# Optimization experiments

Measured on AMD Instinct MI355X. Metric: run time of the kernel, lower is better.

## Reference

```python
import jax, jax.numpy as jnp
import numpy as np

B, N, T, E = 8, 10000, 12, 160000
C_IN, C_SP, C_OUT, K = 32, 64, 64, 3
EPS = 1e-5

def _conv1xk(x, w, b, pad):
    # x: (B, Cin, N, T), w: (Cout, Cin, 1, k) -- conv only along time axis
    y = jax.lax.conv_general_dilated(x, w, (1, 1), [(0, 0), (pad, pad)],
                                     dimension_numbers=('NCHW', 'OIHW', 'NCHW'))
    return y + b[None, :, None, None]

def _temporal_block(x, w, b, gamma, beta, mean, var):
    out = _conv1xk(x, w, b, pad=1)
    p, q = jnp.split(out, 2, axis=1)
    out = p * jax.nn.sigmoid(q)  # GLU gate
    scale = gamma * jax.lax.rsqrt(var + EPS)  # eval-mode BatchNorm2d
    return (out - mean[None, :, None, None]) * scale[None, :, None, None] + beta[None, :, None, None]

def _cheb_conv(x, edge_index, edge_weight, W, b):
    # x: (BT, N, C). PyG ChebConv, sym normalization, lambda_max=2 =>
    # Lhat = -D^{-1/2} A D^{-1/2} (zero diagonal). Recursion T0=x, T1=Lhat x,
    # Tk = 2 Lhat T_{k-1} - T_{k-2}; out = sum_k Tk @ W_k + b.
    row, col = edge_index[0], edge_index[1]
    n = x.shape[1]
    deg = jnp.zeros((n,), x.dtype).at[row].add(edge_weight)
    deg_safe = jnp.where(deg > 0, deg, 1.0)
    dinv = jnp.where(deg > 0, jax.lax.rsqrt(deg_safe), 0.0)
    norm = -edge_weight * dinv[row] * dinv[col]  # (E,)

    def lhat(z):
        msg = z[:, row, :] * norm[None, :, None]          # gather + scale
        return jnp.zeros_like(z).at[:, col, :].add(msg)   # scatter-add

    Tx0 = x
    out = jnp.einsum('bnc,cd->bnd', Tx0, W[0])
    Tx1 = lhat(x)
    out = out + jnp.einsum('bnc,cd->bnd', Tx1, W[1])
    for k in range(2, W.shape[0]):
        Tx2 = 2.0 * lhat(Tx1) - Tx0
        out = out + jnp.einsum('bnc,cd->bnd', Tx2, W[k])
        Tx0, Tx1 = Tx1, Tx2
    return out + b

def setup_inputs():
    key = jax.random.key(0)
    ks = jax.random.split(key, 16)
    s = 0.05
    return {
        'x': jax.random.normal(ks[0], (B, C_IN, N, T), jnp.float32),
        'edge_index': jax.random.randint(ks[1], (2, E), 0, N),
        'edge_weight': jax.random.uniform(ks[2], (E,), jnp.float32),
        'w_gate1': jax.random.normal(ks[3], (2 * C_SP, C_IN, 1, 3), jnp.float32) * s,
        'b_gate1': jnp.zeros((2 * C_SP,), jnp.float32),
        'bn1_gamma': 1.0 + 0.1 * jax.random.normal(ks[4], (C_SP,), jnp.float32),
        'bn1_beta': 0.1 * jax.random.normal(ks[5], (C_SP,), jnp.float32),
        'bn1_mean': 0.1 * jax.random.normal(ks[6], (C_SP,), jnp.float32),
        'bn1_var': jax.random.uniform(ks[7], (C_SP,), jnp.float32, 0.5, 1.5),
        'cheb_w': jax.random.normal(ks[8], (K, C_SP, C_SP), jnp.float32) * s,
        'cheb_b': jnp.zeros((C_SP,), jnp.float32),
        'ln_gamma': jnp.ones((C_SP,), jnp.float32),
        'ln_beta': jnp.zeros((C_SP,), jnp.float32),
        'w_gate2': jax.random.normal(ks[9], (2 * C_OUT, C_SP, 1, 3), jnp.float32) * s,
        'b_gate2': jnp.zeros((2 * C_OUT,), jnp.float32),
        'bn2_gamma': 1.0 + 0.1 * jax.random.normal(ks[10], (C_OUT,), jnp.float32),
        'bn2_beta': 0.1 * jax.random.normal(ks[11], (C_OUT,), jnp.float32),
        'bn2_mean': 0.1 * jax.random.normal(ks[12], (C_OUT,), jnp.float32),
        'bn2_var': jax.random.uniform(ks[13], (C_OUT,), jnp.float32, 0.5, 1.5),
        'w_res': jax.random.normal(ks[14], (C_OUT, C_IN, 1, 1), jnp.float32) * s,
        'b_res': jnp.zeros((C_OUT,), jnp.float32),
    }

def reference(x, edge_index, edge_weight, w_gate1, b_gate1, bn1_gamma, bn1_beta, bn1_mean, bn1_var,
              cheb_w, cheb_b, ln_gamma, ln_beta, w_gate2, b_gate2, bn2_gamma, bn2_beta, bn2_mean,
              bn2_var, w_res, b_res):
    b_, _, n_, t_ = x.shape
    res = _conv1xk(x, w_res, b_res, pad=0)  # 1x1 residual projection
    out = _temporal_block(x, w_gate1, b_gate1, bn1_gamma, bn1_beta, bn1_mean, bn1_var)
    c_s = out.shape[1]
    # (B, C_s, N, T) -> (B*T, N, C_s): spatial graph conv per time snapshot
    h = out.transpose(0, 3, 2, 1).reshape(b_ * t_, n_, c_s)
    h = _cheb_conv(h, edge_index, edge_weight, cheb_w, cheb_b)
    mu = h.mean(-1, keepdims=True)
    var = ((h - mu) ** 2).mean(-1, keepdims=True)
    h = (h - mu) * jax.lax.rsqrt(var + EPS) * ln_gamma + ln_beta  # LayerNorm
    h = jax.nn.relu(h)
    h = h.reshape(b_, t_, n_, c_s).transpose(0, 3, 2, 1)
    out = _temporal_block(h, w_gate2, b_gate2, bn2_gamma, bn2_beta, bn2_mean, bn2_var)
    return out + res
```

## Files before the change

kernel.cpp:

```cpp
#include <hip/hip_runtime.h>
#include <math.h>

#define BB 8
#define CIN 32
#define NN 10000
#define TTT 12
#define EE 160000
#define CSP 64
#define BT (BB*TTT)
#define NPAIR 48
#define EPSV 1e-5f

typedef __attribute__((ext_vector_type(8))) short bf16x8;
typedef __attribute__((ext_vector_type(4))) float f32x4;

static __device__ __forceinline__ float sigmoidf_(float v) {
    return __builtin_amdgcn_rcpf(1.f + __expf(-v));
}

static __device__ __forceinline__ short f2bf(float v) {
    unsigned u = __float_as_uint(v);
    u = (u + 0x7fffu + ((u >> 16) & 1u)) >> 16;
    return (short)u;
}
static __device__ __forceinline__ float lo16f(unsigned u) {
    return __uint_as_float(u << 16);
}
static __device__ __forceinline__ float hi16f(unsigned u) {
    return __uint_as_float(u & 0xffff0000u);
}
static __device__ __forceinline__ unsigned packbf(float a, float b) {
    return ((unsigned)(ushort)f2bf(a)) | (((unsigned)(ushort)f2bf(b)) << 16);
}

__global__ void k_deg(const int* __restrict__ ei, const float* __restrict__ ew,
                      float* __restrict__ deg) {
    int e = blockIdx.x * 256 + threadIdx.x;
    if (e < EE) atomicAdd(&deg[ei[e]], ew[e]);
}

__global__ void k_dinv(float* __restrict__ deg) {
    int n = blockIdx.x * 256 + threadIdx.x;
    if (n < NN) { float d = deg[n]; deg[n] = d > 0.f ? rsqrtf(d) : 0.f; }
}

__global__ void k_norm_cnt(const int* __restrict__ ei, const float* __restrict__ ew,
                           const float* __restrict__ dinv, float* __restrict__ nrm,
                           int* __restrict__ cnt) {
    int e = blockIdx.x * 256 + threadIdx.x;
    if (e < EE) {
        int r = ei[e], c = ei[EE + e];
        nrm[e] = -ew[e] * dinv[r] * dinv[c];
        atomicAdd(&cnt[c], 1);
    }
}

__global__ void k_scan(const int* __restrict__ cnt, int* __restrict__ offs,
                       int* __restrict__ cursor) {
    __shared__ int sh[1024];
    int tid = threadIdx.x;
    int running = 0;
    for (int base = 0; base < NN; base += 1024) {
        int i = base + tid;
        int v = (i < NN) ? cnt[i] : 0;
        sh[tid] = v;
        __syncthreads();
        for (int off = 1; off < 1024; off <<= 1) {
            int t = (tid >= off) ? sh[tid - off] : 0;
            __syncthreads();
            sh[tid] += t;
            __syncthreads();
        }
        int incl = sh[tid];
        if (i < NN) { offs[i] = running + incl - v; cursor[i] = running + incl - v; }
        int ct = sh[1023];
        __syncthreads();
        running += ct;
    }
    if (tid == 0) offs[NN] = running;
}

__global__ void k_fill(const int* __restrict__ ei, const float* __restrict__ nrm,
                       int* __restrict__ cursor, unsigned* __restrict__ csrp) {
    int e = blockIdx.x * 256 + threadIdx.x;
    if (e < EE) {
        int cdst = ei[EE + e];
        int p = atomicAdd(&cursor[cdst], 1);
        csrp[p] = (((unsigned)(ushort)f2bf(nrm[e])) << 16) | (unsigned)ei[e];
    }
}

__global__ void k_cvt_w(const float* __restrict__ wg1, const float* __restrict__ wg2,
                        const float* __restrict__ wr, const float* __restrict__ cwf,
                        short* __restrict__ o1, short* __restrict__ o2,
                        short* __restrict__ o3, short* __restrict__ wt02,
                        short* __restrict__ wt1, short* __restrict__ wt2) {
    int i = blockIdx.x * 256 + threadIdx.x;
    if (i < 12288) o1[i] = f2bf(wg1[i]);
    if (i < 24576) o2[i] = f2bf(wg2[i]);
    if (i < 2048)  o3[i] = f2bf(wr[i]);
    if (i < 4096) {
        int cout = i >> 6, cin = i & 63;
        float w0 = cwf[cin * 64 + cout];
        float w1 = cwf[4096 + cin * 64 + cout];
        float w2 = cwf[8192 + cin * 64 + cout];
        wt02[i] = f2bf(w0 - w2);
        wt1[i]  = f2bf(w1);
        wt2[i]  = f2bf(w2);
    }
}

__global__ __launch_bounds__(256, 4) void k_tconv1_mfma(
    const float* __restrict__ x, const short* __restrict__ wbf,
    const float* __restrict__ bg, const float* __restrict__ gam,
    const float* __restrict__ bet, const float* __restrict__ mean,
    const float* __restrict__ var, ushort* __restrict__ h1)
{
    __shared__ short Btl[3 * 48 * 40];
    int bi = blockIdx.x;
    int b = bi / 2500;
    int n0 = (bi % 2500) * 4;
    int tid = threadIdx.x;

    for (int j = tid; j < 384; j += 256) {
        int ci = j / 12, r = j - ci * 12;
        const float* xp = x + ((size_t)(b * CIN + ci) * NN + n0) * 12 + r * 4;
        float4 v = *(const float4*)xp;
        float vv[4] = {v.x, v.y, v.z, v.w};
#pragma unroll
        for (int e = 0; e < 4; ++e) {
            int at = r * 4 + e;
            int n = at / 12, t = at - n * 12;
            short bv = f2bf(vv[e]);
#pragma unroll
            for (int kk = 0; kk < 3; ++kk) {
                int tp = t + 1 - kk;
                if (tp >= 0 && tp < 12) {
                    int K = ci * 3 + kk;
                    Btl[((K >> 5) * 48 + n * 12 + tp) * 40 + (K & 31)] = bv;
                }
            }
            if (t == 0)  { int K = ci * 3;     Btl[((K >> 5) * 48 + n * 12) * 40 + (K & 31)] = 0; }
            if (t == 11) { int K = ci * 3 + 2; Btl[((K >> 5) * 48 + n * 12 + 11) * 40 + (K & 31)] = 0; }
        }
    }
    __syncthreads();

    int w = tid >> 6, l = tid & 63, lr = l & 15, lq = l >> 4;
    f32x4 aP[3], aQ[3];
#pragma unroll
    for (int m = 0; m < 3; ++m) { aP[m] = (f32x4){0,0,0,0}; aQ[m] = (f32x4){0,0,0,0}; }

#pragma unroll
    for (int ks = 0; ks < 3; ++ks) {
        bf16x8 wp = *(const bf16x8*)(wbf + ((w * 16 + lr) * 96 + ks * 32 + lq * 8));
        bf16x8 wq = *(const bf16x8*)(wbf + ((64 + w * 16 + lr) * 96 + ks * 32 + lq * 8));
#pragma unroll
        for (int mt = 0; mt < 3; ++mt) {
            bf16x8 im = *(const bf16x8*)(&Btl[(ks * 48 + mt * 16 + lr) * 40 + lq * 8]);
            aP[mt] = __builtin_amdgcn_mfma_f32_16x16x32_bf16(im, wp, aP[mt], 0, 0, 0);
            aQ[mt] = __builtin_amdgcn_mfma_f32_16x16x32_bf16(im, wq, aQ[mt], 0, 0, 0);
        }
    }

    int c = w * 16 + lr;
    float bp = bg[c], bq = bg[64 + c];
    float sc = gam[c] * rsqrtf(var[c] + EPSV);
    float mn = mean[c], be = bet[c];
#pragma unroll
    for (int mt = 0; mt < 3; ++mt) {
#pragma unroll
        for (int j = 0; j < 4; ++j) {
            int row = mt * 16 + lq * 4 + j;
            int n = n0 + row / 12, t = row % 12;
            float h = (aP[mt][j] + bp) * sigmoidf_(aQ[mt][j] + bq);
            h1[((size_t)(b * 6 + (t >> 1)) * NN + n) * 128 + (t & 1) * 64 + c] =
                (ushort)f2bf((h - mn) * sc + be);
        }
    }
}

__global__ __launch_bounds__(256, 8) void k_spatial(
    const ushort* __restrict__ h1, const int* __restrict__ offs,
    const unsigned* __restrict__ csr,
    const short* __restrict__ wt02, const short* __restrict__ wt1,
    const short* __restrict__ wt2, const float* __restrict__ cb,
    ushort* __restrict__ O, ushort* __restrict__ U)
{
    __shared__ short Al[64][72];
    __shared__ short Gl[64][72];
    int tid = threadIdx.x;
    int bi = blockIdx.x;
    int xcd = bi & 7, r = bi >> 3;
    int jp = r / 313, ck = r - jp * 313;
    int pair = xcd * 6 + jp;
    int n0 = ck * 32;

    const char* hp = (const char*)h1 + (size_t)pair * NN * 256;
    int w = tid >> 6, l = tid & 63;
    int snap = l >> 5, cp = l & 31;
    unsigned loff = (unsigned)(snap * 128 + cp * 4);

#pragma unroll
    for (int p = 0; p < 8; ++p) {
        int nl = p * 4 + w;
        int n = n0 + nl;
        float a0 = 0.f, a1 = 0.f, b0 = 0.f, b1 = 0.f;
        unsigned sv = 0;
        if (n < NN) {
            sv = *(const unsigned*)(hp + (((unsigned)n) << 8) + loff);
            int o0 = __builtin_amdgcn_readfirstlane(offs[n]);
            int o1 = __builtin_amdgcn_readfirstlane(offs[n + 1]);
            int i = o0;
            for (; i + 3 < o1; i += 4) {
                unsigned e0 = csr[i], e1 = csr[i + 1], e2 = csr[i + 2], e3 = csr[i + 3];
                unsigned r0 = *(const unsigned*)(hp + ((e0 & 0xffffu) << 8) + loff);
                unsigned r1 = *(const unsigned*)(hp + ((e1 & 0xffffu) << 8) + loff);
                unsigned r2 = *(const unsigned*)(hp + ((e2 & 0xffffu) << 8) + loff);
                unsigned r3 = *(const unsigned*)(hp + ((e3 & 0xffffu) << 8) + loff);
                float w0 = hi16f(e0), w1 = hi16f(e1), w2 = hi16f(e2), w3 = hi16f(e3);
                a0 = fmaf(w0, lo16f(r0), a0); a1 = fmaf(w0, hi16f(r0), a1);
                b0 = fmaf(w1, lo16f(r1), b0); b1 = fmaf(w1, hi16f(r1), b1);
                a0 = fmaf(w2, lo16f(r2), a0); a1 = fmaf(w2, hi16f(r2), a1);
                b0 = fmaf(w3, lo16f(r3), b0); b1 = fmaf(w3, hi16f(r3), b1);
            }
            for (; i < o1; ++i) {
                unsigned e = csr[i];
                unsigned rr = *(const unsigned*)(hp + ((e & 0xffffu) << 8) + loff);
                float ww = hi16f(e);
                a0 = fmaf(ww, lo16f(rr), a0); a1 = fmaf(ww, hi16f(rr), a1);
            }
        }
        int row = snap * 32 + nl;
        *(unsigned*)&Al[row][cp * 2] = sv;
        *(unsigned*)&Gl[row][cp * 2] = packbf(a0 + b0, a1 + b1);
    }
    __syncthreads();

    int lr = l & 15, lq = l >> 4;
    bf16x8 af[2], gf[2];
#pragma unroll
    for (int ks = 0; ks < 2; ++ks) {
        af[ks] = *(const bf16x8*)&Al[w * 16 + lr][ks * 32 + lq * 8];
        gf[ks] = *(const bf16x8*)&Gl[w * 16 + lr][ks * 32 + lq * 8];
    }
    f32x4 ao[4], au[4];
#pragma unroll
    for (int ct = 0; ct < 4; ++ct) { ao[ct] = (f32x4){0,0,0,0}; au[ct] = (f32x4){0,0,0,0}; }
#pragma unroll
    for (int ct = 0; ct < 4; ++ct) {
#pragma unroll
        for (int ks = 0; ks < 2; ++ks) {
            int woff = (ct * 16 + lr) * 64 + ks * 32 + lq * 8;
            bf16x8 b02 = *(const bf16x8*)(wt02 + woff);
            bf16x8 b1  = *(const bf16x8*)(wt1 + woff);
            bf16x8 b2  = *(const bf16x8*)(wt2 + woff);
            ao[ct] = __builtin_amdgcn_mfma_f32_16x16x32_bf16(af[ks], b02, ao[ct], 0, 0, 0);
            ao[ct] = __builtin_amdgcn_mfma_f32_16x16x32_bf16(gf[ks], b1,  ao[ct], 0, 0, 0);
            au[ct] = __builtin_amdgcn_mfma_f32_16x16x32_bf16(gf[ks], b2,  au[ct], 0, 0, 0);
        }
    }
    __syncthreads();

#pragma unroll
    for (int ct = 0; ct < 4; ++ct) {
        float bb = cb[ct * 16 + lr];
#pragma unroll
        for (int j2 = 0; j2 < 4; ++j2) {
            int rowo = w * 16 + lq * 4 + j2;
            Al[rowo][ct * 16 + lr] = f2bf(ao[ct][j2] + bb);
            Gl[rowo][ct * 16 + lr] = f2bf(au[ct][j2]);
        }
    }
    __syncthreads();

    size_t obase = (size_t)pair * NN * 128;
#pragma unroll
    for (int rr = 0; rr < 2; ++rr) {
        int idx = tid + rr * 256;
        int node = idx >> 4, part = idx & 15;
        int sn = part >> 3, seg = part & 7;
        int n = n0 + node;
        if (n < NN) {
            size_t off = obase + (size_t)n * 128 + sn * 64 + seg * 8;
            __builtin_nontemporal_store(*(const bf16x8*)&Al[sn * 32 + node][seg * 8],
                                        (bf16x8*)(O + off));
            __builtin_nontemporal_store(*(const bf16x8*)&Gl[sn * 32 + node][seg * 8],
                                        (bf16x8*)(U + off));
        }
    }
}

__global__ __launch_bounds__(256, 8) void k_gather2_ln(
    const ushort* __restrict__ O, const ushort* __restrict__ U,
    const int* __restrict__ offs, const unsigned* __restrict__ csr,
    const float* __restrict__ lng, const float* __restrict__ lnb,
    ushort* __restrict__ hln)
{
    int bi = blockIdx.x;
    int xcd = bi & 7, r = bi >> 3;
    int jp = r / 625, ck = r - jp * 625;
    int pair = xcd * 6 + jp;
    int ng = ck * 16;
    int tid = threadIdx.x;
    int w = tid >> 6, l = tid & 63;
    int snap = l >> 5, cp = l & 31;
    unsigned loff = (unsigned)(snap * 128 + cp * 4);
    const char* up = (const char*)U + (size_t)pair * NN * 256;
    const char* op = (const char*)O + (size_t)pair * NN * 256;
    ushort* hlp = hln + (size_t)pair * NN * 128;

    float2 gv = ((const float2*)lng)[cp];
    float2 bv = ((const float2*)lnb)[cp];

#pragma unroll
    for (int p = 0; p < 4; ++p) {
        int n = ng + p * 4 + w;
        float a0 = 0.f, a1 = 0.f, b0 = 0.f, b1 = 0.f;
        int o0 = __builtin_amdgcn_readfirstlane(offs[n]);
        int o1 = __builtin_amdgcn_readfirstlane(offs[n + 1]);
        int i = o0;
        for (; i + 3 < o1; i += 4) {
            unsigned e0 = csr[i], e1 = csr[i + 1], e2 = csr[i + 2], e3 = csr[i + 3];
            unsigned r0 = *(const unsigned*)(up + ((e0 & 0xffffu) << 8) + loff);
            unsigned r1 = *(const unsigned*)(up + ((e1 & 0xffffu) << 8) + loff);
            unsigned r2 = *(const unsigned*)(up + ((e2 & 0xffffu) << 8) + loff);
            unsigned r3 = *(const unsigned*)(up + ((e3 & 0xffffu) << 8) + loff);
            float w0 = hi16f(e0), w1 = hi16f(e1), w2 = hi16f(e2), w3 = hi16f(e3);
            a0 = fmaf(w0, lo16f(r0), a0); a1 = fmaf(w0, hi16f(r0), a1);
            b0 = fmaf(w1, lo16f(r1), b0); b1 = fmaf(w1, hi16f(r1), b1);
            a0 = fmaf(w2, lo16f(r2), a0); a1 = fmaf(w2, hi16f(r2), a1);
            b0 = fmaf(w3, lo16f(r3), b0); b1 = fmaf(w3, hi16f(r3), b1);
        }
        for (; i < o1; ++i) {
            unsigned e = csr[i];
            unsigned rr = *(const unsigned*)(up + ((e & 0xffffu) << 8) + loff);
            float ww = hi16f(e);
            a0 = fmaf(ww, lo16f(rr), a0); a1 = fmaf(ww, hi16f(rr), a1);
        }
        unsigned ov = *(const unsigned*)(op + (((unsigned)n) << 8) + loff);
        float acc0 = lo16f(ov) + 2.f * (a0 + b0);
        float acc1 = hi16f(ov) + 2.f * (a1 + b1);
        float s1 = acc0 + acc1;
        float s2 = acc0 * acc0 + acc1 * acc1;
#pragma unroll
        for (int m = 16; m >= 1; m >>= 1) {
            s1 += __shfl_xor(s1, m);
            s2 += __shfl_xor(s2, m);
        }
        float mu = s1 * (1.f / 64.f);
        float vr = s2 * (1.f / 64.f) - mu * mu;
        float rstd = rsqrtf(vr + EPSV);
        float y0 = fmaxf((acc0 - mu) * rstd * gv.x + bv.x, 0.f);
        float y1 = fmaxf((acc1 - mu) * rstd * gv.y + bv.y, 0.f);
        __builtin_nontemporal_store(packbf(y0, y1),
            (unsigned*)(hlp + (size_t)n * 128 + snap * 64 + cp * 2));
    }
}

__global__ __launch_bounds__(256, 4) void k_tconv2_mfma(
    const ushort* __restrict__ hln, const float* __restrict__ x,
    const short* __restrict__ wbf, const short* __restrict__ wrbf,
    const float* __restrict__ bg, const float* __restrict__ gam,
    const float* __restrict__ bet, const float* __restrict__ mean,
    const float* __restrict__ var, const float* __restrict__ bres,
    float* __restrict__ out)
{
    __shared__ short Btl[6 * 48 * 40];
    __shared__ short Bx[48 * 40];
    int bi = blockIdx.x;
    int b = bi / 2500;
    int n0 = (bi % 2500) * 4;
    int tid = threadIdx.x;

    {
        int n = tid >> 6, c = tid & 63;
#pragma unroll
        for (int t = 0; t < 12; ++t) {
            short bv = (short)hln[((size_t)(b * 6 + (t >> 1)) * NN + n0 + n) * 128 +
                                  (t & 1) * 64 + c];
#pragma unroll
            for (int kk = 0; kk < 3; ++kk) {
                int tp = t + 1 - kk;
                if (tp >= 0 && tp < 12) {
                    int K = c * 3 + kk;
                    Btl[((K >> 5) * 48 + n * 12 + tp) * 40 + (K & 31)] = bv;
                }
            }
            if (t == 0)  { int K = c * 3;     Btl[((K >> 5) * 48 + n * 12) * 40 + (K & 31)] = 0; }
            if (t == 11) { int K = c * 3 + 2; Btl[((K >> 5) * 48 + n * 12 + 11) * 40 + (K & 31)] = 0; }
        }
    }
    for (int j = tid; j < 384; j += 256) {
        int ci = j / 12, r = j - ci * 12;
        const float* xp = x + ((size_t)(b * CIN + ci) * NN + n0) * 12 + r * 4;
        float4 v = *(const float4*)xp;
        float vv[4] = {v.x, v.y, v.z, v.w};
#pragma unroll
        for (int e = 0; e < 4; ++e) {
            int col = r * 4 + e;
            Bx[col * 40 + ci] = f2bf(vv[e]);
        }
    }
    __syncthreads();

    int w = tid >> 6, l = tid & 63, lr = l & 15, lq = l >> 4;
    f32x4 accP[3], accQ[3], accR[3];
#pragma unroll
    for (int m = 0; m < 3; ++m) {
        accP[m] = (f32x4){0,0,0,0}; accQ[m] = (f32x4){0,0,0,0}; accR[m] = (f32x4){0,0,0,0};
    }

#pragma unroll
    for (int ks = 0; ks < 6; ++ks) {
        bf16x8 aP = *(const bf16x8*)(wbf + ((w * 16 + lr) * 192 + ks * 32 + lq * 8));
        bf16x8 aQ = *(const bf16x8*)(wbf + ((64 + w * 16 + lr) * 192 + ks * 32 + lq * 8));
#pragma unroll
        for (int ct = 0; ct < 3; ++ct) {
            bf16x8 bfr = *(const bf16x8*)(&Btl[(ks * 48 + ct * 16 + lr) * 40 + lq * 8]);
            accP[ct] = __builtin_amdgcn_mfma_f32_16x16x32_bf16(aP, bfr, accP[ct], 0, 0, 0);
            accQ[ct] = __builtin_amdgcn_mfma_f32_16x16x32_bf16(aQ, bfr, accQ[ct], 0, 0, 0);
        }
    }
    {
        bf16x8 aR = *(const bf16x8*)(wrbf + ((w * 16 + lr) * 32 + lq * 8));
#pragma unroll
        for (int ct = 0; ct < 3; ++ct) {
            bf16x8 bx = *(const bf16x8*)(&Bx[(ct * 16 + lr) * 40 + lq * 8]);
            accR[ct] = __builtin_amdgcn_mfma_f32_16x16x32_bf16(aR, bx, accR[ct], 0, 0, 0);
        }
    }

    float bpv[4], bqv[4], scv[4], mnv[4], bev[4], brv[4];
#pragma unroll
    for (int j = 0; j < 4; ++j) {
        int cj = w * 16 + lq * 4 + j;
        bpv[j] = bg[cj]; bqv[j] = bg[64 + cj];
        scv[j] = gam[cj] * rsqrtf(var[cj] + EPSV);
        mnv[j] = mean[cj]; bev[j] = bet[cj]; brv[j] = bres[cj];
    }
#pragma unroll
    for (int ct = 0; ct < 3; ++ct) {
        int col = ct * 16 + lr;
        int n = n0 + col / 12, t = col % 12;
#pragma unroll
        for (int j = 0; j < 4; ++j) {
            int cj = w * 16 + lq * 4 + j;
            float h = (accP[ct][j] + bpv[j]) * sigmoidf_(accQ[ct][j] + bqv[j]);
            float o = (h - mnv[j]) * scv[j] + bev[j] + accR[ct][j] + brv[j];
            __builtin_nontemporal_store(o, &out[((size_t)(b * 64 + cj) * NN + n) * 12 + t]);
        }
    }
}

extern "C" void kernel_launch(void* const* d_in, const int* in_sizes, int n_in,
                              void* d_out, int out_size, void* d_ws, size_t ws_size,
                              hipStream_t stream)
{
    const float* x   = (const float*)d_in[0];
    const int*   ei  = (const int*)d_in[1];
    const float* ew  = (const float*)d_in[2];
    const float* wg1 = (const float*)d_in[3];
    const float* bg1 = (const float*)d_in[4];
    const float* g1  = (const float*)d_in[5];
    const float* be1 = (const float*)d_in[6];
    const float* m1  = (const float*)d_in[7];
    const float* v1  = (const float*)d_in[8];
    const float* cw  = (const float*)d_in[9];
    const float* cb  = (const float*)d_in[10];
    const float* lng = (const float*)d_in[11];
    const float* lnb = (const float*)d_in[12];
    const float* wg2 = (const float*)d_in[13];
    const float* bg2 = (const float*)d_in[14];
    const float* g2  = (const float*)d_in[15];
    const float* be2 = (const float*)d_in[16];
    const float* m2  = (const float*)d_in[17];
    const float* v2  = (const float*)d_in[18];
    const float* wr  = (const float*)d_in[19];
    const float* br  = (const float*)d_in[20];

    char* w = (char*)d_ws;
    short* wbf1  = (short*)w;  w += 12288 * 2;
    short* wbf2  = (short*)w;  w += 24576 * 2;
    short* wrbf  = (short*)w;  w += 2048 * 2;
    short* wt02  = (short*)w;  w += 4096 * 2;
    short* wt1   = (short*)w;  w += 4096 * 2;
    short* wt2   = (short*)w;  w += 4096 * 2;
    ushort* h1   = (ushort*)w; w += (size_t)NPAIR * NN * 128 * 2;
    ushort* O    = (ushort*)w; w += (size_t)NPAIR * NN * 128 * 2;
    float* deg   = (float*)w;  w += NN * 4;
    int*   cnt   = (int*)w;    w += NN * 4;
    int*   offs  = (int*)w;    w += (NN + 1) * 4;
    int*   cursor= (int*)w;    w += NN * 4;
    float* nrm   = (float*)w;  w += EE * 4;
    unsigned* csr = (unsigned*)w; w += EE * 4;
    ushort* U = (ushort*)d_out;

    hipMemsetAsync(deg, 0, NN * 4 * 2, stream);

    k_deg<<<625, 256, 0, stream>>>(ei, ew, deg);
    k_dinv<<<40, 256, 0, stream>>>(deg);
    k_norm_cnt<<<625, 256, 0, stream>>>(ei, ew, deg, nrm, cnt);
    k_scan<<<1, 1024, 0, stream>>>(cnt, offs, cursor);
    k_fill<<<625, 256, 0, stream>>>(ei, nrm, cursor, csr);
    k_cvt_w<<<96, 256, 0, stream>>>(wg1, wg2, wr, cw, wbf1, wbf2, wrbf, wt02, wt1, wt2);

    k_tconv1_mfma<<<BB * 2500, 256, 0, stream>>>(x, wbf1, bg1, g1, be1, m1, v1, h1);
    k_spatial<<<8 * 6 * 313, 256, 0, stream>>>(h1, offs, csr, wt02, wt1, wt2, cb, O, U);
    k_gather2_ln<<<8 * 6 * 625, 256, 0, stream>>>(O, U, offs, csr, lng, lnb, h1);
    k_tconv2_mfma<<<BB * 2500, 256, 0, stream>>>(h1, x, wbf2, wrbf, bg2, g2, be2, m2, v2, br,
                                                 (float*)d_out);
}
```

Baseline: 894.8 us.

## Stage padded time tiles in LDS and index conv taps directly, unroll gathers by 8

Both temporal conv kernels no longer expand inputs into an im2col tile in LDS. They stage a zero-padded (node, time+2, channel) tile and reorder the weights per tap so each MFMA B-operand reads a shifted row directly. This cuts redundant LDS writes and scattered short stores, and in tconv2 it allows vectorized 16-byte loads of h1. The sparse gather loops in the spatial and gather2 kernels are also unrolled to 8 edges for more memory-level parallelism, at the cost of more registers. tconv1 launch bounds go from 4 to 6 blocks per CU.

Result: faster. 818.5 us (-8.5%).

```diff
diff --git a/kernel.cpp b/kernel.cpp
--- a/kernel.cpp
+++ b/kernel.cpp
@@ -92,12 +92,18 @@
 
 __global__ void k_cvt_w(const float* __restrict__ wg1, const float* __restrict__ wg2,
                         const float* __restrict__ wr, const float* __restrict__ cwf,
-                        short* __restrict__ o1, short* __restrict__ o2,
+                        short* __restrict__ wtap1, short* __restrict__ wtap2,
                         short* __restrict__ o3, short* __restrict__ wt02,
                         short* __restrict__ wt1, short* __restrict__ wt2) {
     int i = blockIdx.x * 256 + threadIdx.x;
-    if (i < 12288) o1[i] = f2bf(wg1[i]);
-    if (i < 24576) o2[i] = f2bf(wg2[i]);
+    if (i < 12288) {
+        int kk = i / 4096, r = i % 4096, cc = r >> 5, ci = r & 31;
+        wtap1[i] = f2bf(wg1[cc * 96 + ci * 3 + kk]);
+    }
+    if (i < 24576) {
+        int kk = i / 8192, r = i % 8192, cc = r >> 6, c = r & 63;
+        wtap2[i] = f2bf(wg2[cc * 192 + c * 3 + kk]);
+    }
     if (i < 2048)  o3[i] = f2bf(wr[i]);
     if (i < 4096) {
         int cout = i >> 6, cin = i & 63;
@@ -110,56 +116,53 @@
     }
 }
 
-__global__ __launch_bounds__(256, 4) void k_tconv1_mfma(
-    const float* __restrict__ x, const short* __restrict__ wbf,
+__global__ __launch_bounds__(256, 6) void k_tconv1_mfma(
+    const float* __restrict__ x, const short* __restrict__ wtap,
     const float* __restrict__ bg, const float* __restrict__ gam,
     const float* __restrict__ bet, const float* __restrict__ mean,
     const float* __restrict__ var, ushort* __restrict__ h1)
 {
-    __shared__ short Btl[3 * 48 * 40];
+    __shared__ short Hs[4][14][40];
     int bi = blockIdx.x;
     int b = bi / 2500;
     int n0 = (bi % 2500) * 4;
     int tid = threadIdx.x;
 
-    for (int j = tid; j < 384; j += 256) {
-        int ci = j / 12, r = j - ci * 12;
-        const float* xp = x + ((size_t)(b * CIN + ci) * NN + n0) * 12 + r * 4;
-        float4 v = *(const float4*)xp;
-        float vv[4] = {v.x, v.y, v.z, v.w};
-#pragma unroll
-        for (int e = 0; e < 4; ++e) {
-            int at = r * 4 + e;
-            int n = at / 12, t = at - n * 12;
-            short bv = f2bf(vv[e]);
-#pragma unroll
-            for (int kk = 0; kk < 3; ++kk) {
-                int tp = t + 1 - kk;
-                if (tp >= 0 && tp < 12) {
-                    int K = ci * 3 + kk;
-                    Btl[((K >> 5) * 48 + n * 12 + tp) * 40 + (K & 31)] = bv;
-                }
-            }
-            if (t == 0)  { int K = ci * 3;     Btl[((K >> 5) * 48 + n * 12) * 40 + (K & 31)] = 0; }
-            if (t == 11) { int K = ci * 3 + 2; Btl[((K >> 5) * 48 + n * 12 + 11) * 40 + (K & 31)] = 0; }
-        }
+    if (tid < 128) {
+        int n = tid >> 5, ci = tid & 31;
+        const float* xp = x + ((size_t)(b * CIN + ci) * NN + n0 + n) * 12;
+        float4 a0 = *(const float4*)(xp);
+        float4 a1 = *(const float4*)(xp + 4);
+        float4 a2 = *(const float4*)(xp + 8);
+        short* d = &Hs[n][0][ci];
+        d[0] = 0; d[13 * 40] = 0;
+        d[1 * 40] = f2bf(a0.x); d[2 * 40] = f2bf(a0.y); d[3 * 40] = f2bf(a0.z);
+        d[4 * 40] = f2bf(a0.w); d[5 * 40] = f2bf(a1.x); d[6 * 40] = f2bf(a1.y);
+        d[7 * 40] = f2bf(a1.z); d[8 * 40] = f2bf(a1.w); d[9 * 40] = f2bf(a2.x);
+        d[10 * 40] = f2bf(a2.y); d[11 * 40] = f2bf(a2.z); d[12 * 40] = f2bf(a2.w);
     }
     __syncthreads();
 
     int w = tid >> 6, l = tid & 63, lr = l & 15, lq = l >> 4;
+    int nct[3], tct[3];
+#pragma unroll
+    for (int ct = 0; ct < 3; ++ct) {
+        int col = ct * 16 + lr;
+        nct[ct] = col / 12; tct[ct] = col % 12;
+    }
     f32x4 aP[3], aQ[3];
 #pragma unroll
     for (int m = 0; m < 3; ++m) { aP[m] = (f32x4){0,0,0,0}; aQ[m] = (f32x4){0,0,0,0}; }
 
 #pragma unroll
-    for (int ks = 0; ks < 3; ++ks) {
-        bf16x8 wp = *(const bf16x8*)(wbf + ((w * 16 + lr) * 96 + ks * 32 + lq * 8));
-        bf16x8 wq = *(const bf16x8*)(wbf + ((64 + w * 16 + lr) * 96 + ks * 32 + lq * 8));
-#pragma unroll
-        for (int mt = 0; mt < 3; ++mt) {
-            bf16x8 im = *(const bf16x8*)(&Btl[(ks * 48 + mt * 16 + lr) * 40 + lq * 8]);
-            aP[mt] = __builtin_amdgcn_mfma_f32_16x16x32_bf16(im, wp, aP[mt], 0, 0, 0);
-            aQ[mt] = __builtin_amdgcn_mfma_f32_16x16x32_bf16(im, wq, aQ[mt], 0, 0, 0);
+    for (int kk = 0; kk < 3; ++kk) {
+        bf16x8 wp = *(const bf16x8*)(wtap + ((kk * 128 + w * 16 + lr) * 32 + lq * 8));
+        bf16x8 wq = *(const bf16x8*)(wtap + ((kk * 128 + 64 + w * 16 + lr) * 32 + lq * 8));
+#pragma unroll
+        for (int ct = 0; ct < 3; ++ct) {
+            bf16x8 im = *(const bf16x8*)&Hs[nct[ct]][tct[ct] + kk][lq * 8];
+            aP[ct] = __builtin_amdgcn_mfma_f32_16x16x32_bf16(im, wp, aP[ct], 0, 0, 0);
+            aQ[ct] = __builtin_amdgcn_mfma_f32_16x16x32_bf16(im, wq, aQ[ct], 0, 0, 0);
         }
     }
 
@@ -212,8 +215,30 @@
             int o0 = __builtin_amdgcn_readfirstlane(offs[n]);
             int o1 = __builtin_amdgcn_readfirstlane(offs[n + 1]);
             int i = o0;
+            for (; i + 7 < o1; i += 8) {
+                unsigned e0 = csr[i], e1 = csr[i+1], e2 = csr[i+2], e3 = csr[i+3];
+                unsigned e4 = csr[i+4], e5 = csr[i+5], e6 = csr[i+6], e7 = csr[i+7];
+                unsigned r0 = *(const unsigned*)(hp + ((e0 & 0xffffu) << 8) + loff);
+                unsigned r1 = *(const unsigned*)(hp + ((e1 & 0xffffu) << 8) + loff);
+                unsigned r2 = *(const unsigned*)(hp + ((e2 & 0xffffu) << 8) + loff);
+                unsigned r3 = *(const unsigned*)(hp + ((e3 & 0xffffu) << 8) + loff);
+                unsigned r4 = *(const unsigned*)(hp + ((e4 & 0xffffu) << 8) + loff);
+                unsigned r5 = *(const unsigned*)(hp + ((e5 & 0xffffu) << 8) + loff);
+                unsigned r6 = *(const unsigned*)(hp + ((e6 & 0xffffu) << 8) + loff);
+                unsigned r7 = *(const unsigned*)(hp + ((e7 & 0xffffu) << 8) + loff);
+                float w0 = hi16f(e0), w1 = hi16f(e1), w2 = hi16f(e2), w3 = hi16f(e3);
+                float w4 = hi16f(e4), w5 = hi16f(e5), w6 = hi16f(e6), w7 = hi16f(e7);
+                a0 = fmaf(w0, lo16f(r0), a0); a1 = fmaf(w0, hi16f(r0), a1);
+                b0 = fmaf(w1, lo16f(r1), b0); b1 = fmaf(w1, hi16f(r1), b1);
+                a0 = fmaf(w2, lo16f(r2), a0); a1 = fmaf(w2, hi16f(r2), a1);
+                b0 = fmaf(w3, lo16f(r3), b0); b1 = fmaf(w3, hi16f(r3), b1);
+                a0 = fmaf(w4, lo16f(r4), a0); a1 = fmaf(w4, hi16f(r4), a1);
+                b0 = fmaf(w5, lo16f(r5), b0); b1 = fmaf(w5, hi16f(r5), b1);
+                a0 = fmaf(w6, lo16f(r6), a0); a1 = fmaf(w6, hi16f(r6), a1);
+                b0 = fmaf(w7, lo16f(r7), b0); b1 = fmaf(w7, hi16f(r7), b1);
+            }
             for (; i + 3 < o1; i += 4) {
-                unsigned e0 = csr[i], e1 = csr[i + 1], e2 = csr[i + 2], e3 = csr[i + 3];
+                unsigned e0 = csr[i], e1 = csr[i+1], e2 = csr[i+2], e3 = csr[i+3];
                 unsigned r0 = *(const unsigned*)(hp + ((e0 & 0xffffu) << 8) + loff);
                 unsigned r1 = *(const unsigned*)(hp + ((e1 & 0xffffu) << 8) + loff);
                 unsigned r2 = *(const unsigned*)(hp + ((e2 & 0xffffu) << 8) + loff);
@@ -276,8 +301,8 @@
 
     size_t obase = (size_t)pair * NN * 128;
 #pragma unroll
-    for (int rr = 0; rr < 2; ++rr) {
-        int idx = tid + rr * 256;
+    for (int rr2 = 0; rr2 < 2; ++rr2) {
+        int idx = tid + rr2 * 256;
         int node = idx >> 4, part = idx & 15;
         int sn = part >> 3, seg = part & 7;
         int n = n0 + node;
@@ -320,8 +345,30 @@
         int o0 = __builtin_amdgcn_readfirstlane(offs[n]);
         int o1 = __builtin_amdgcn_readfirstlane(offs[n + 1]);
         int i = o0;
+        for (; i + 7 < o1; i += 8) {
+            unsigned e0 = csr[i], e1 = csr[i+1], e2 = csr[i+2], e3 = csr[i+3];
+            unsigned e4 = csr[i+4], e5 = csr[i+5], e6 = csr[i+6], e7 = csr[i+7];
+            unsigned r0 = *(const unsigned*)(up + ((e0 & 0xffffu) << 8) + loff);
+            unsigned r1 = *(const unsigned*)(up + ((e1 & 0xffffu) << 8) + loff);
+            unsigned r2 = *(const unsigned*)(up + ((e2 & 0xffffu) << 8) + loff);
+            unsigned r3 = *(const unsigned*)(up + ((e3 & 0xffffu) << 8) + loff);
+            unsigned r4 = *(const unsigned*)(up + ((e4 & 0xffffu) << 8) + loff);
+            unsigned r5 = *(const unsigned*)(up + ((e5 & 0xffffu) << 8) + loff);
+            unsigned r6 = *(const unsigned*)(up + ((e6 & 0xffffu) << 8) + loff);
+            unsigned r7 = *(const unsigned*)(up + ((e7 & 0xffffu) << 8) + loff);
+            float w0 = hi16f(e0), w1 = hi16f(e1), w2 = hi16f(e2), w3 = hi16f(e3);
+            float w4 = hi16f(e4), w5 = hi16f(e5), w6 = hi16f(e6), w7 = hi16f(e7);
+            a0 = fmaf(w0, lo16f(r0), a0); a1 = fmaf(w0, hi16f(r0), a1);
+            b0 = fmaf(w1, lo16f(r1), b0); b1 = fmaf(w1, hi16f(r1), b1);
+            a0 = fmaf(w2, lo16f(r2), a0); a1 = fmaf(w2, hi16f(r2), a1);
+            b0 = fmaf(w3, lo16f(r3), b0); b1 = fmaf(w3, hi16f(r3), b1);
+            a0 = fmaf(w4, lo16f(r4), a0); a1 = fmaf(w4, hi16f(r4), a1);
+            b0 = fmaf(w5, lo16f(r5), b0); b1 = fmaf(w5, hi16f(r5), b1);
+            a0 = fmaf(w6, lo16f(r6), a0); a1 = fmaf(w6, hi16f(r6), a1);
+            b0 = fmaf(w7, lo16f(r7), b0); b1 = fmaf(w7, hi16f(r7), b1);
+        }
         for (; i + 3 < o1; i += 4) {
-            unsigned e0 = csr[i], e1 = csr[i + 1], e2 = csr[i + 2], e3 = csr[i + 3];
+            unsigned e0 = csr[i], e1 = csr[i+1], e2 = csr[i+2], e3 = csr[i+3];
             unsigned r0 = *(const unsigned*)(up + ((e0 & 0xffffu) << 8) + loff);
             unsigned r1 = *(const unsigned*)(up + ((e1 & 0xffffu) << 8) + loff);
             unsigned r2 = *(const unsigned*)(up + ((e2 & 0xffffu) << 8) + loff);
@@ -360,36 +407,29 @@
 
 __global__ __launch_bounds__(256, 4) void k_tconv2_mfma(
     const ushort* __restrict__ hln, const float* __restrict__ x,
-    const short* __restrict__ wbf, const short* __restrict__ wrbf,
+    const short* __restrict__ wtap, const short* __restrict__ wrbf,
     const float* __restrict__ bg, const float* __restrict__ gam,
     const float* __restrict__ bet, const float* __restrict__ mean,
     const float* __restrict__ var, const float* __restrict__ bres,
     float* __restrict__ out)
 {
-    __shared__ short Btl[6 * 48 * 40];
+    __shared__ short Hs[4][14][72];
     __shared__ short Bx[48 * 40];
     int bi = blockIdx.x;
     int b = bi / 2500;
     int n0 = (bi % 2500) * 4;
     int tid = threadIdx.x;
 
-    {
-        int n = tid >> 6, c = tid & 63;
-#pragma unroll
-        for (int t = 0; t < 12; ++t) {
-            short bv = (short)hln[((size_t)(b * 6 + (t >> 1)) * NN + n0 + n) * 128 +
-                                  (t & 1) * 64 + c];
-#pragma unroll
-            for (int kk = 0; kk < 3; ++kk) {
-                int tp = t + 1 - kk;
-                if (tp >= 0 && tp < 12) {
-                    int K = c * 3 + kk;
-                    Btl[((K >> 5) * 48 + n * 12 + tp) * 40 + (K & 31)] = bv;
-                }
-            }
-            if (t == 0)  { int K = c * 3;     Btl[((K >> 5) * 48 + n * 12) * 40 + (K & 31)] = 0; }
-            if (t == 11) { int K = c * 3 + 2; Btl[((K >> 5) * 48 + n * 12 + 11) * 40 + (K & 31)] = 0; }
-        }
+    for (int j = tid; j < 384; j += 256) {
+        int n = j / 96, rem = j % 96;
+        int p = rem >> 4, seg = rem & 15;
+        bf16x8 v = *(const bf16x8*)(hln + ((size_t)(b * 6 + p) * NN + n0 + n) * 128 + seg * 8);
+        *(bf16x8*)&Hs[n][1 + 2 * p + (seg >> 3)][(seg & 7) * 8] = v;
+    }
+    if (tid < 64) {
+        int n = tid >> 4, pt = tid & 15;
+        bf16x8 z = (bf16x8){0,0,0,0,0,0,0,0};
+        *(bf16x8*)&Hs[n][(pt >> 3) * 13][(pt & 7) * 8] = z;
     }
     for (int j = tid; j < 384; j += 256) {
         int ci = j / 12, r = j - ci * 12;
@@ -405,6 +445,12 @@
     __syncthreads();
 
     int w = tid >> 6, l = tid & 63, lr = l & 15, lq = l >> 4;
+    int nct[3], tct[3];
+#pragma unroll
+    for (int ct = 0; ct < 3; ++ct) {
+        int col = ct * 16 + lr;
+        nct[ct] = col / 12; tct[ct] = col % 12;
+    }
     f32x4 accP[3], accQ[3], accR[3];
 #pragma unroll
     for (int m = 0; m < 3; ++m) {
@@ -412,14 +458,17 @@
     }
 
 #pragma unroll
-    for (int ks = 0; ks < 6; ++ks) {
-        bf16x8 aP = *(const bf16x8*)(wbf + ((w * 16 + lr) * 192 + ks * 32 + lq * 8));
-        bf16x8 aQ = *(const bf16x8*)(wbf + ((64 + w * 16 + lr) * 192 + ks * 32 + lq * 8));
-#pragma unroll
-        for (int ct = 0; ct < 3; ++ct) {
-            bf16x8 bfr = *(const bf16x8*)(&Btl[(ks * 48 + ct * 16 + lr) * 40 + lq * 8]);
-            accP[ct] = __builtin_amdgcn_mfma_f32_16x16x32_bf16(aP, bfr, accP[ct], 0, 0, 0);
-            accQ[ct] = __builtin_amdgcn_mfma_f32_16x16x32_bf16(aQ, bfr, accQ[ct], 0, 0, 0);
+    for (int kk = 0; kk < 3; ++kk) {
+#pragma unroll
+        for (int ks = 0; ks < 2; ++ks) {
+            bf16x8 aP = *(const bf16x8*)(wtap + ((kk * 128 + w * 16 + lr) * 64 + ks * 32 + lq * 8));
+            bf16x8 aQ = *(const bf16x8*)(wtap + ((kk * 128 + 64 + w * 16 + lr) * 64 + ks * 32 + lq * 8));
+#pragma unroll
+            for (int ct = 0; ct < 3; ++ct) {
+                bf16x8 bfr = *(const bf16x8*)&Hs[nct[ct]][tct[ct] + kk][ks * 32 + lq * 8];
+                accP[ct] = __builtin_amdgcn_mfma_f32_16x16x32_bf16(aP, bfr, accP[ct], 0, 0, 0);
+                accQ[ct] = __builtin_amdgcn_mfma_f32_16x16x32_bf16(aQ, bfr, accQ[ct], 0, 0, 0);
+            }
         }
     }
     {
@@ -480,8 +529,8 @@
     const float* br  = (const float*)d_in[20];
 
     char* w = (char*)d_ws;
-    short* wbf1  = (short*)w;  w += 12288 * 2;
-    short* wbf2  = (short*)w;  w += 24576 * 2;
+    short* wtap1 = (short*)w;  w += 12288 * 2;
+    short* wtap2 = (short*)w;  w += 24576 * 2;
     short* wrbf  = (short*)w;  w += 2048 * 2;
     short* wt02  = (short*)w;  w += 4096 * 2;
     short* wt1   = (short*)w;  w += 4096 * 2;
@@ -503,11 +552,11 @@
     k_norm_cnt<<<625, 256, 0, stream>>>(ei, ew, deg, nrm, cnt);
     k_scan<<<1, 1024, 0, stream>>>(cnt, offs, cursor);
     k_fill<<<625, 256, 0, stream>>>(ei, nrm, cursor, csr);
-    k_cvt_w<<<96, 256, 0, stream>>>(wg1, wg2, wr, cw, wbf1, wbf2, wrbf, wt02, wt1, wt2);
-
-    k_tconv1_mfma<<<BB * 2500, 256, 0, stream>>>(x, wbf1, bg1, g1, be1, m1, v1, h1);
+    k_cvt_w<<<96, 256, 0, stream>>>(wg1, wg2, wr, cw, wtap1, wtap2, wrbf, wt02, wt1, wt2);
+
+    k_tconv1_mfma<<<BB * 2500, 256, 0, stream>>>(x, wtap1, bg1, g1, be1, m1, v1, h1);
     k_spatial<<<8 * 6 * 313, 256, 0, stream>>>(h1, offs, csr, wt02, wt1, wt2, cb, O, U);
     k_gather2_ln<<<8 * 6 * 625, 256, 0, stream>>>(O, U, offs, csr, lng, lnb, h1);
-    k_tconv2_mfma<<<BB * 2500, 256, 0, stream>>>(h1, x, wbf2, wrbf, bg2, g2, be2, m2, v2, br,
+    k_tconv2_mfma<<<BB * 2500, 256, 0, stream>>>(h1, x, wtap2, wrbf, bg2, g2, be2, m2, v2, br,
                                                  (float*)d_out);
 }
```
